# Optimization experiments

Hardware: AMD Instinct MI355X
Metric: run time of the kernel (lower is better)

## Reference

```python
import jax, jax.numpy as jnp
import numpy as np

H_OUT, W_OUT = 473, 473  # original image size the logits are upsampled to
BN_EPS = 1e-5


def _conv(x, w, pad):
    return jax.lax.conv_general_dilated(
        x, w, window_strides=(1, 1), padding=[(pad, pad), (pad, pad)],
        dimension_numbers=('NCHW', 'OIHW', 'NCHW'))


def _bn(x, g, b):
    # BatchNorm2d in training mode: batch statistics over (N, H, W)
    m = jnp.mean(x, axis=(0, 2, 3), keepdims=True)
    v = jnp.var(x, axis=(0, 2, 3), keepdims=True)
    return (x - m) * jax.lax.rsqrt(v + BN_EPS) * g.reshape(1, -1, 1, 1) + b.reshape(1, -1, 1, 1)


def setup_inputs() -> dict:
    key = jax.random.key(0)
    ks = jax.random.split(key, 8)
    B, C, Hf, Wf, NC = 2, 256, 60, 60, 2
    return {
        'V_a': jax.random.normal(ks[0], (B, C, Hf, Wf), jnp.float32),
        'V_b': jax.random.normal(ks[1], (B, C, Hf, Wf), jnp.float32),
        'D_a': jax.random.normal(ks[2], (B, C, Hf, Wf), jnp.float32),
        'W_e': jax.random.normal(ks[3], (C, C), jnp.float32) * 0.02,
        'gate_w': jax.random.normal(ks[4], (1, C, 1, 1), jnp.float32) * 0.01,
        'conv1_w': jax.random.normal(ks[5], (C, 3 * C, 3, 3), jnp.float32) * 0.01,
        'conv2_w': jax.random.normal(ks[6], (C, 2 * C, 3, 3), jnp.float32) * 0.01,
        'bn1_g': jnp.ones((C,), jnp.float32),
        'bn1_b': jnp.zeros((C,), jnp.float32),
        'bn2_g': jnp.ones((C,), jnp.float32),
        'bn2_b': jnp.zeros((C,), jnp.float32),
        'cls1_w': jax.random.normal(ks[7], (NC, C, 1, 1), jnp.float32) * 0.01,
        'cls1_b': jnp.zeros((NC,), jnp.float32),
        'cls2_w': jax.random.normal(jax.random.fold_in(key, 9), (NC, C, 1, 1), jnp.float32) * 0.01,
        'cls2_b': jnp.zeros((NC,), jnp.float32),
    }


def reference(V_a, V_b, D_a, W_e, gate_w, conv1_w, conv2_w,
              bn1_g, bn1_b, bn2_g, bn2_b, cls1_w, cls1_b, cls2_w, cls2_b):
    B, C, Hf, Wf = V_a.shape
    N = Hf * Wf
    V_a_flat = V_a.reshape(B, C, N)
    V_b_flat = V_b.reshape(B, C, N)

    # linear_e on transposed A features, then affinity S = (A^T W^T) B
    weighted = jnp.einsum('bcn,dc->bnd', V_a_flat, W_e)        # [B, N, C]
    S = jnp.einsum('bnd,bdm->bnm', weighted, V_b_flat)         # [B, N, N]

    S_row = jax.nn.softmax(S, axis=1)                          # softmax over dim 1
    S_colT = jax.nn.softmax(jnp.swapaxes(S, 1, 2), axis=1)     # softmax of S^T over dim 1

    Z_b = jnp.einsum('bcn,bnm->bcm', V_a_flat, S_row)          # attended for view b
    Z_a = jnp.einsum('bcn,bnm->bcm', V_b_flat, S_colT)         # attended for view a

    att1 = Z_a.reshape(B, C, Hf, Wf)
    att2 = Z_b.reshape(B, C, Hf, Wf)

    # 1x1 sigmoid gates
    att1 = att1 * jax.nn.sigmoid(_conv(att1, gate_w, 0))
    att2 = att2 * jax.nn.sigmoid(_conv(att2, gate_w, 0))

    # conc1: branch-1 concatenates gated attention, RGB feat, and depth feat
    x1 = jnp.concatenate([att1, V_a, D_a], axis=1)             # [B, 3C, Hf, Wf]
    x2 = jnp.concatenate([att2, V_b], axis=1)                  # [B, 2C, Hf, Wf]

    x1 = jax.nn.relu(_bn(_conv(x1, conv1_w, 1), bn1_g, bn1_b))
    x2 = jax.nn.relu(_bn(_conv(x2, conv2_w, 1), bn2_g, bn2_b))

    x1 = _conv(x1, cls1_w, 0) + cls1_b.reshape(1, -1, 1, 1)
    x2 = _conv(x2, cls2_w, 0) + cls2_b.reshape(1, -1, 1, 1)

    NC = cls1_w.shape[0]
    x1 = jax.image.resize(x1, (B, NC, H_OUT, W_OUT), 'linear')
    x2 = jax.image.resize(x2, (B, NC, H_OUT, W_OUT), 'linear')
    return jax.nn.sigmoid(x1), jax.nn.sigmoid(x2)
```

## Files before the change

### kernel.cpp

```cpp
#include <hip/hip_runtime.h>

#define BB 2
#define CC 256
#define NN 3600
#define NCH 2
#define HO 473
#define WO 473
#define NP 3648
#define NR 3712
#define LDT 72
#define NTI 29
#define ZKS 6

typedef unsigned short u16;
typedef __attribute__((ext_vector_type(8))) short short8;
typedef __attribute__((ext_vector_type(4))) float f32x4;

static __device__ __forceinline__ u16 f2bf(float f) {
    unsigned u = __float_as_uint(f);
    unsigned r = (u + 0x7FFF + ((u >> 16) & 1)) >> 16;
    return (u16)r;
}
static __device__ __forceinline__ u16 f2h(float f) {
    _Float16 h = (_Float16)f;
    return __builtin_bit_cast(unsigned short, h);
}
static __device__ __forceinline__ float h2f(u16 u) {
    _Float16 h = __builtin_bit_cast(_Float16, u);
    return (float)h;
}

__global__ __launch_bounds__(256)
void gemm_we(const u16* __restrict__ vat, const u16* __restrict__ web,
             u16* __restrict__ wgtb)
{
    __shared__ u16 As[128 * LDT];
    __shared__ u16 Bs[128 * LDT];
    const u16* A = vat + (long)blockIdx.z * NR * CC;
    u16* Cp = wgtb + (long)blockIdx.z * NR * CC;

    const int t = threadIdx.x;
    const int w = t >> 6, lane = t & 63;
    const int mh = (w >> 1) * 64, nh = (w & 1) * 64;
    const int lm = lane & 15, quad = lane >> 4;
    const int m0 = blockIdx.y * 128, n0 = blockIdx.x * 128;

    f32x4 acc[4][4] = {};

    for (int k0 = 0; k0 < CC; k0 += 64) {
#pragma unroll
        for (int i = 0; i < 4; ++i) {
            int idx = i * 256 + t;
            int row = idx >> 3, c8 = (idx & 7) * 8;
            int rg = m0 + row;
            uint4 v = make_uint4(0u, 0u, 0u, 0u);
            if (rg < NN) v = *(const uint4*)(A + (long)rg * CC + k0 + c8);
            *(uint4*)(&As[row * LDT + c8]) = v;
            uint4 bv = make_uint4(0u, 0u, 0u, 0u);
            if (n0 + row < CC) bv = *(const uint4*)(web + (long)(n0 + row) * CC + k0 + c8);
            *(uint4*)(&Bs[row * LDT + c8]) = bv;
        }
        __syncthreads();
#pragma unroll
        for (int s = 0; s < 2; ++s) {
            short8 a[4], b[4];
#pragma unroll
            for (int i = 0; i < 4; ++i)
                a[i] = *(const short8*)(&As[(mh + i * 16 + lm) * LDT + s * 32 + quad * 8]);
#pragma unroll
            for (int j = 0; j < 4; ++j)
                b[j] = *(const short8*)(&Bs[(nh + j * 16 + lm) * LDT + s * 32 + quad * 8]);
#pragma unroll
            for (int i = 0; i < 4; ++i)
#pragma unroll
                for (int j = 0; j < 4; ++j)
                    acc[i][j] = __builtin_amdgcn_mfma_f32_16x16x32_bf16(a[i], b[j], acc[i][j], 0, 0, 0);
        }
        __syncthreads();
    }
#pragma unroll
    for (int i = 0; i < 4; ++i)
#pragma unroll
        for (int r = 0; r < 4; ++r) {
            int row = m0 + mh + i * 16 + quad * 4 + r;
            if (row < NN)
#pragma unroll
                for (int j = 0; j < 4; ++j) {
                    int col = n0 + nh + j * 16 + lm;
                    if (col < CC) Cp[(long)row * CC + col] = f2bf(acc[i][j][r]);
                }
        }
}

__global__ __launch_bounds__(256)
void gemm_s_stats(const u16* __restrict__ A, const u16* __restrict__ B,
                  u16* __restrict__ Sh, u16* __restrict__ STh,
                  float* __restrict__ prowm, float* __restrict__ prows,
                  float* __restrict__ pcolm, float* __restrict__ pcols)
{
    __shared__ u16 smem[2 * 128 * LDT];
    u16* As = smem;
    u16* Bs = smem + 128 * LDT;

    const int t = threadIdx.x;
    const int w = t >> 6, lane = t & 63;
    const int mh = (w >> 1) * 64, nh = (w & 1) * 64;
    const int lm = lane & 15, quad = lane >> 4;
    const int m0 = blockIdx.y * 128, n0 = blockIdx.x * 128;

    f32x4 acc[4][4] = {};

    for (int k0 = 0; k0 < CC; k0 += 64) {
#pragma unroll
        for (int i = 0; i < 4; ++i) {
            int idx = i * 256 + t;
            int row = idx >> 3, c8 = (idx & 7) * 8;
            uint4 v = make_uint4(0u, 0u, 0u, 0u);
            if (m0 + row < NN) v = *(const uint4*)(A + (long)(m0 + row) * CC + k0 + c8);
            *(uint4*)(&As[row * LDT + c8]) = v;
            uint4 bv = make_uint4(0u, 0u, 0u, 0u);
            if (n0 + row < NN) bv = *(const uint4*)(B + (long)(n0 + row) * CC + k0 + c8);
            *(uint4*)(&Bs[row * LDT + c8]) = bv;
        }
        __syncthreads();
#pragma unroll
        for (int s = 0; s < 2; ++s) {
            short8 a[4], b[4];
#pragma unroll
            for (int i = 0; i < 4; ++i)
                a[i] = *(const short8*)(&As[(mh + i * 16 + lm) * LDT + s * 32 + quad * 8]);
#pragma unroll
            for (int j = 0; j < 4; ++j)
                b[j] = *(const short8*)(&Bs[(nh + j * 16 + lm) * LDT + s * 32 + quad * 8]);
#pragma unroll
            for (int i = 0; i < 4; ++i)
#pragma unroll
                for (int j = 0; j < 4; ++j)
                    acc[i][j] = __builtin_amdgcn_mfma_f32_16x16x32_bf16(a[i], b[j], acc[i][j], 0, 0, 0);
        }
        __syncthreads();
    }

#pragma unroll
    for (int i = 0; i < 4; ++i)
#pragma unroll
        for (int r = 0; r < 4; ++r) {
            int row = m0 + mh + i * 16 + quad * 4 + r;
            if (row < NN)
#pragma unroll
                for (int j = 0; j < 4; ++j) {
                    int col = n0 + nh + j * 16 + lm;
                    if (col < NN) Sh[(long)row * NP + col] = f2h(acc[i][j][r]);
                }
        }

    bool cval[4];
#pragma unroll
    for (int j = 0; j < 4; ++j) cval[j] = (n0 + nh + j * 16 + lm) < NN;

    float* sm = (float*)smem;
    float* rowm = sm;
    float* rows_ = sm + 256;
    float* colm = sm + 512;
    float* cols_ = sm + 768;
    __syncthreads();

#pragma unroll
    for (int i = 0; i < 4; ++i)
#pragma unroll
        for (int r = 0; r < 4; ++r) {
            float m = -3.0e38f;
#pragma unroll
            for (int j = 0; j < 4; ++j) if (cval[j]) m = fmaxf(m, acc[i][j][r]);
            m = fmaxf(m, __shfl_xor(m, 1, 64));
            m = fmaxf(m, __shfl_xor(m, 2, 64));
            m = fmaxf(m, __shfl_xor(m, 4, 64));
            m = fmaxf(m, __shfl_xor(m, 8, 64));
            float s = 0.f;
#pragma unroll
            for (int j = 0; j < 4; ++j) if (cval[j]) s += __expf(acc[i][j][r] - m);
            s += __shfl_xor(s, 1, 64);
            s += __shfl_xor(s, 2, 64);
            s += __shfl_xor(s, 4, 64);
            s += __shfl_xor(s, 8, 64);
            if (lm == 0) {
                int rr = mh + i * 16 + quad * 4 + r;
                rowm[(w & 1) * 128 + rr] = m;
                rows_[(w & 1) * 128 + rr] = s;
            }
        }

#pragma unroll
    for (int j = 0; j < 4; ++j) {
        float m = -3.0e38f;
#pragma unroll
        for (int i = 0; i < 4; ++i)
#pragma unroll
            for (int r = 0; r < 4; ++r)
                if (m0 + mh + i * 16 + quad * 4 + r < NN) m = fmaxf(m, acc[i][j][r]);
        m = fmaxf(m, __shfl_xor(m, 16, 64));
        m = fmaxf(m, __shfl_xor(m, 32, 64));
        float s = 0.f;
#pragma unroll
        for (int i = 0; i < 4; ++i)
#pragma unroll
            for (int r = 0; r < 4; ++r)
                if (m0 + mh + i * 16 + quad * 4 + r < NN) s += __expf(acc[i][j][r] - m);
        s += __shfl_xor(s, 16, 64);
        s += __shfl_xor(s, 32, 64);
        if (quad == 0) {
            int ccl = nh + j * 16 + lm;
            colm[(w >> 1) * 128 + ccl] = m;
            cols_[(w >> 1) * 128 + ccl] = s;
        }
    }
    __syncthreads();

    if (t < 128) {
        float m1 = rowm[t], m2 = rowm[128 + t];
        float M = fmaxf(m1, m2);
        float s = rows_[t] * __expf(m1 - M) + rows_[128 + t] * __expf(m2 - M);
        if (m0 + t < NN) {
            prowm[(long)blockIdx.x * NR + m0 + t] = M;
            prows[(long)blockIdx.x * NR + m0 + t] = s;
        }
    } else {
        int c = t - 128;
        float m1 = colm[c], m2 = colm[128 + c];
        float M = fmaxf(m1, m2);
        float s = cols_[c] * __expf(m1 - M) + cols_[128 + c] * __expf(m2 - M);
        if (n0 + c < NN) {
            pcolm[(long)blockIdx.y * NR + n0 + c] = M;
            pcols[(long)blockIdx.y * NR + n0 + c] = s;
        }
    }

    __syncthreads();
    u16* tr = smem;
#pragma unroll
    for (int i = 0; i < 4; ++i)
#pragma unroll
        for (int j = 0; j < 4; ++j)
#pragma unroll
            for (int r = 0; r < 4; ++r)
                tr[(nh + j * 16 + lm) * 136 + (mh + i * 16 + quad * 4 + r)] = f2h(acc[i][j][r]);
    __syncthreads();
    {
        int row = t >> 1, hf = t & 1;
        int mg = n0 + row;
        if (mg < NN) {
#pragma unroll
            for (int q = 0; q < 8; ++q) {
                int cb = m0 + hf * 64 + q * 8;
                if (cb < NN)
                    *(uint4*)(&STh[(long)mg * NP + cb]) =
                        *(const uint4*)(&tr[row * 136 + hf * 64 + q * 8]);
            }
        }
    }
}

__global__ __launch_bounds__(256)
void stats_combine(const float* __restrict__ prowm, const float* __restrict__ prows,
                   const float* __restrict__ pcolm, const float* __restrict__ pcols,
                   float* __restrict__ rmx, float* __restrict__ rsm,
                   float* __restrict__ cmx, float* __restrict__ csm)
{
    int i = blockIdx.x * 256 + threadIdx.x;
    if (i >= NN) return;
    const float* pm = blockIdx.y ? pcolm : prowm;
    const float* ps = blockIdx.y ? pcols : prows;
    float m = -3.0e38f, s = 0.f;
#pragma unroll 4
    for (int tI = 0; tI < NTI; ++tI) {
        float m2 = pm[(long)tI * NR + i], s2 = ps[(long)tI * NR + i];
        float M = fmaxf(m, m2);
        s = s * __expf(m - M) + s2 * __expf(m2 - M);
        m = M;
    }
    if (blockIdx.y) { cmx[i] = m; csm[i] = s; }
    else            { rmx[i] = m; rsm[i] = s; }
}

__global__ __launch_bounds__(256)
void p_build(u16* __restrict__ Sh, u16* __restrict__ STh,
             const float* __restrict__ rmx, const float* __restrict__ rsm,
             const float* __restrict__ cmx, const float* __restrict__ csm)
{
    int r = blockIdx.x;
    u16* M = blockIdx.y ? STh : Sh;
    const float* mx = blockIdx.y ? cmx : rmx;
    const float* sm = blockIdx.y ? csm : rsm;
    float mv = mx[r];
    float inv = 1.f / sm[r];
    u16* row = M + (long)r * NP;
    int t = threadIdx.x;
    for (int c0 = t * 8; c0 < NP; c0 += 2048) {
        uint4 hv = *(const uint4*)(row + c0);
        const u16* hp = (const u16*)&hv;
        u16 o[8];
#pragma unroll
        for (int e = 0; e < 8; ++e) {
            int c = c0 + e;
            o[e] = (c < NN) ? f2bf(__expf(h2f(hp[e]) - mv) * inv) : (u16)0;
        }
        *(uint4*)(row + c0) = *(const uint4*)o;
    }
}

__global__ __launch_bounds__(256, 4)
void gemm_z_128(const u16* __restrict__ vab_b, const u16* __restrict__ vbb_b,
                const u16* __restrict__ PT, const u16* __restrict__ P,
                float* __restrict__ Zb_b, float* __restrict__ Za_b)
{
    __shared__ u16 As[128 * LDT];
    __shared__ u16 Bs[128 * LDT];

    const int t = threadIdx.x;
    const int w = t >> 6, lane = t & 63;
    const int mh = (w >> 1) * 64, nh = (w & 1) * 64;
    const int lm = lane & 15, quad = lane >> 4;
    const int n0 = blockIdx.x * 128;
    const int ks = blockIdx.y;
    const int zz = blockIdx.z;
    const int branch = zz & 1;
    const int m0 = (zz >> 1) * 128;
    const u16* A = branch ? vbb_b : vab_b;
    const u16* B = branch ? P : PT;
    float* Cp = branch ? Za_b : Zb_b;

    const int base = 57 / ZKS, rem = 57 % ZKS;
    const int it0 = ks * base + (ks < rem ? ks : rem);
    const int itn = base + (ks < rem ? 1 : 0);

    f32x4 acc[4][4] = {};

    for (int it = it0; it < it0 + itn; ++it) {
        const int k0 = it * 64;
#pragma unroll
        for (int i = 0; i < 4; ++i) {
            int idx = i * 256 + t;
            int row = idx >> 3, c8 = (idx & 7) * 8;
            uint4 v = *(const uint4*)(A + (long)(m0 + row) * NP + k0 + c8);
            *(uint4*)(&As[row * LDT + c8]) = v;
            int rg = n0 + row;
            uint4 bv = make_uint4(0u, 0u, 0u, 0u);
            if (rg < NN) bv = *(const uint4*)(B + (long)rg * NP + k0 + c8);
            *(uint4*)(&Bs[row * LDT + c8]) = bv;
        }
        __syncthreads();
#pragma unroll
        for (int s = 0; s < 2; ++s) {
            short8 a[4], b[4];
#pragma unroll
            for (int i = 0; i < 4; ++i)
                a[i] = *(const short8*)(&As[(mh + i * 16 + lm) * LDT + s * 32 + quad * 8]);
#pragma unroll
            for (int j = 0; j < 4; ++j)
                b[j] = *(const short8*)(&Bs[(nh + j * 16 + lm) * LDT + s * 32 + quad * 8]);
#pragma unroll
            for (int i = 0; i < 4; ++i)
#pragma unroll
                for (int j = 0; j < 4; ++j)
                    acc[i][j] = __builtin_amdgcn_mfma_f32_16x16x32_bf16(a[i], b[j], acc[i][j], 0, 0, 0);
        }
        __syncthreads();
    }

#pragma unroll
    for (int i = 0; i < 4; ++i)
#pragma unroll
        for (int r = 0; r < 4; ++r) {
            int row = m0 + mh + i * 16 + quad * 4 + r;
#pragma unroll
            for (int j = 0; j < 4; ++j) {
                int col = n0 + nh + j * 16 + lm;
                if (col < NN)
                    atomicAdd(&Cp[(long)row * NN + col], acc[i][j][r]);
            }
        }
}

__global__ __launch_bounds__(256, 4)
void conv_both(const u16* __restrict__ W1, const u16* __restrict__ W2,
               const u16* __restrict__ gzaT, const u16* __restrict__ vat,
               const u16* __restrict__ daT, const u16* __restrict__ gzbT,
               const u16* __restrict__ vbt,
               float* __restrict__ y1, float* __restrict__ y2)
{
    __shared__ u16 As[128 * LDT];
    __shared__ u16 Bs[128 * LDT];

    const int t = threadIdx.x;
    const int w = t >> 6, lane = t & 63;
    const int mh = (w >> 1) * 64, nh = (w & 1) * 64;
    const int lm = lane & 15, quad = lane >> 4;

    const long L = blockIdx.x + (long)NTI * (blockIdx.y + (long)ZKS * blockIdx.z);
    const int combo = (int)(L & 7);
    const long rest = L >> 3;
    const int ks = (int)(rest % ZKS);
    const int px = (int)(rest / ZKS);
    const int which = combo >> 2;
    const int b = (combo >> 1) & 1;
    const int m0 = (combo & 1) * 128;
    const int n0 = px * 128;

    const int CIN = which ? 512 : 768;
    const int KT = 9 * CIN;
    const u16* W = which ? W2 : W1;
    const u16* P0 = which ? gzbT : gzaT;
    const u16* P1 = which ? vbt : vat;
    const u16* P2 = which ? vbt : daT;
    float* Y = which ? y2 : y1;
    const long pstride = (long)NR * CC;

    const int per = (KT / 64) / ZKS;
    const int it0 = ks * per;

    f32x4 acc[4][4] = {};

    for (int it = it0; it < it0 + per; ++it) {
        const int k0 = it * 64;
        int tap = k0 / CIN;
        int kloc = k0 - tap * CIN;
        int plane = kloc >> 8, cip = kloc & 255;
        int dh = tap / 3 - 1, dw = tap - (tap / 3) * 3 - 1;
        int off = dh * 60 + dw;
        const u16* src = (plane == 0) ? P0 : ((plane == 1) ? P1 : P2);
        src += (long)b * pstride + cip;

#pragma unroll
        for (int i = 0; i < 4; ++i) {
            int idx = i * 256 + t;
            int row = idx >> 3, c8 = (idx & 7) * 8;
            uint4 v = *(const uint4*)(W + (long)(m0 + row) * KT + k0 + c8);
            *(uint4*)(&As[row * LDT + c8]) = v;
            int p = n0 + row;
            uint4 bv = make_uint4(0u, 0u, 0u, 0u);
            if (p < NN) {
                int h = p / 60, wp = p - h * 60;
                int hh = h + dh, wq = wp + dw;
                if (hh >= 0 && hh < 60 && wq >= 0 && wq < 60)
                    bv = *(const uint4*)(src + (long)(p + off) * CC + c8);
            }
            *(uint4*)(&Bs[row * LDT + c8]) = bv;
        }
        __syncthreads();
#pragma unroll
        for (int s = 0; s < 2; ++s) {
            short8 a[4], bfr[4];
#pragma unroll
            for (int i = 0; i < 4; ++i)
                a[i] = *(const short8*)(&As[(mh + i * 16 + lm) * LDT + s * 32 + quad * 8]);
#pragma unroll
            for (int j = 0; j < 4; ++j)
                bfr[j] = *(const short8*)(&Bs[(nh + j * 16 + lm) * LDT + s * 32 + quad * 8]);
#pragma unroll
            for (int i = 0; i < 4; ++i)
#pragma unroll
                for (int j = 0; j < 4; ++j)
                    acc[i][j] = __builtin_amdgcn_mfma_f32_16x16x32_bf16(a[i], bfr[j], acc[i][j], 0, 0, 0);
        }
        __syncthreads();
    }

    float* out = Y + (long)b * CC * NN;
#pragma unroll
    for (int i = 0; i < 4; ++i)
#pragma unroll
        for (int r = 0; r < 4; ++r) {
            int row = m0 + mh + i * 16 + quad * 4 + r;
#pragma unroll
            for (int j = 0; j < 4; ++j) {
                int col = n0 + nh + j * 16 + lm;
                if (col < NN)
                    atomicAdd(&out[(long)row * NN + col], acc[i][j][r]);
            }
        }
}

__global__ __launch_bounds__(256)
void cvt_we(const float* __restrict__ W, u16* __restrict__ O)
{
    int i = blockIdx.x * 256 + threadIdx.x;
    if (i < CC * CC) O[i] = f2bf(W[i]);
}

__global__ __launch_bounds__(256)
void transpose_cvt(const float* __restrict__ V, u16* __restrict__ VT,
                   u16* __restrict__ Vpad)
{
    __shared__ float tile[64][65];
    int b = blockIdx.z, c0 = blockIdx.y * 64, n0 = blockIdx.x * 64;
    int t = threadIdx.x;
#pragma unroll
    for (int e = 0; e < 16; ++e) {
        int f = e * 256 + t; int i = f >> 6, j = f & 63;
        int n = n0 + j;
        float v = 0.f;
        if (n < NN) v = V[((long)b * CC + c0 + i) * NN + n];
        tile[i][j] = v;
        if (Vpad) Vpad[((long)b * CC + c0 + i) * NP + n] = f2bf(v);
    }
    __syncthreads();
#pragma unroll
    for (int e = 0; e < 16; ++e) {
        int f = e * 256 + t; int i = f >> 6, j = f & 63;
        int n = n0 + i;
        if (n < NN) VT[((long)b * NR + n) * CC + c0 + j] = f2bf(tile[j][i]);
    }
}

__global__ __launch_bounds__(256)
void transpose_gate(const float* __restrict__ Z, const float* __restrict__ sg,
                    u16* __restrict__ ZT)
{
    __shared__ float tile[64][65];
    int b = blockIdx.z, c0 = blockIdx.y * 64, n0 = blockIdx.x * 64;
    int t = threadIdx.x;
#pragma unroll
    for (int e = 0; e < 16; ++e) {
        int f = e * 256 + t; int i = f >> 6, j = f & 63;
        int n = n0 + j;
        float v = 0.f;
        if (n < NN) v = Z[((long)b * CC + c0 + i) * NN + n];
        tile[i][j] = v;
    }
    __syncthreads();
#pragma unroll
    for (int e = 0; e < 16; ++e) {
        int f = e * 256 + t; int i = f >> 6, j = f & 63;
        int n = n0 + i;
        if (n < NN)
            ZT[((long)b * NR + n) * CC + c0 + j] = f2bf(tile[j][i] * sg[b * NN + n]);
    }
}

template<int CIN>
__global__ __launch_bounds__(256)
void cvt_convw(const float* __restrict__ W, u16* __restrict__ O)
{
    const int KT = 9 * CIN;
    long idx = (long)blockIdx.x * 256 + threadIdx.x;
    if (idx >= (long)CC * KT) return;
    int co = (int)(idx / KT);
    int r = (int)(idx % KT);
    int tap = r / CIN, ci = r % CIN;
    O[idx] = f2bf(W[((long)co * CIN + ci) * 9 + tap]);
}

__global__ __launch_bounds__(256)
void gate_sig(const float* __restrict__ Z, const float* __restrict__ gw,
              float* __restrict__ sg)
{
    int t = threadIdx.x;
    int px = t & 63, ck = t >> 6;
    int b = blockIdx.y;
    int p = blockIdx.x * 64 + px;
    const float* Zp = Z + (long)b * CC * NN;
    float g = 0.f;
    if (p < NN) {
        for (int c = ck * 64; c < ck * 64 + 64; ++c) g += gw[c] * Zp[(long)c * NN + p];
    }
    __shared__ float red[256];
    red[t] = g;
    __syncthreads();
    if (t < 64) {
        int pp = blockIdx.x * 64 + t;
        if (pp < NN) {
            float tot = red[t] + red[t + 64] + red[t + 128] + red[t + 192];
            sg[b * NN + pp] = 1.f / (1.f + __expf(-tot));
        }
    }
}

__global__ __launch_bounds__(256)
void bn_stats_kernel(const float* __restrict__ Y, const float* __restrict__ g,
                     const float* __restrict__ beta, float* __restrict__ scale,
                     float* __restrict__ shift)
{
    int c = blockIdx.x, t = threadIdx.x;
    float s = 0.f, sq = 0.f;
    for (int b = 0; b < BB; ++b) {
        const float* p = Y + (long)b * CC * NN + (long)c * NN;
        for (int i = t; i < NN; i += 256) { float v = p[i]; s += v; sq += v * v; }
    }
    __shared__ float ls[256], lq[256];
    ls[t] = s; lq[t] = sq;
    __syncthreads();
    for (int off = 128; off > 0; off >>= 1) {
        if (t < off) { ls[t] += ls[t + off]; lq[t] += lq[t + off]; }
        __syncthreads();
    }
    if (t == 0) {
        const float inv = 1.f / (float)(BB * NN);
        float mean = ls[0] * inv;
        float var = fmaxf(lq[0] * inv - mean * mean, 0.f);
        float sc = g[c] * rsqrtf(var + 1e-5f);
        scale[c] = sc;
        shift[c] = beta[c] - mean * sc;
    }
}

__global__ __launch_bounds__(256)
void cls_kernel(const float* __restrict__ Y, const float* __restrict__ scale,
                const float* __restrict__ shift, const float* __restrict__ cw,
                const float* __restrict__ cb, float* __restrict__ O)
{
    int t = threadIdx.x;
    int px = t & 63, ck = t >> 6;
    int b = blockIdx.y;
    int p = blockIdx.x * 64 + px;
    const float* Yb = Y + (long)b * CC * NN;
    float a0 = 0.f, a1 = 0.f;
    if (p < NN) {
        for (int c = ck * 64; c < ck * 64 + 64; ++c) {
            float v = Yb[(long)c * NN + p] * scale[c] + shift[c];
            v = fmaxf(v, 0.f);
            a0 += cw[c] * v;
            a1 += cw[CC + c] * v;
        }
    }
    __shared__ float r0[256], r1[256];
    r0[t] = a0; r1[t] = a1;
    __syncthreads();
    if (t < 64) {
        int pp = blockIdx.x * 64 + t;
        if (pp < NN) {
            float s0 = r0[t] + r0[t + 64] + r0[t + 128] + r0[t + 192];
            float s1 = r1[t] + r1[t + 64] + r1[t + 128] + r1[t + 192];
            O[(long)b * NCH * NN + pp] = s0 + cb[0];
            O[(long)b * NCH * NN + NN + pp] = s1 + cb[1];
        }
    }
}

__global__ __launch_bounds__(256)
void resize_sig_kernel(const float* __restrict__ I1, const float* __restrict__ I2,
                       float* __restrict__ O)
{
    const long HALF = (long)BB * NCH * HO * WO;
    long gid = (long)blockIdx.x * 256 + threadIdx.x;
    if (gid >= HALF) return;
    int half = blockIdx.y;
    const float* I = half ? I2 : I1;
    float* Op = O + half * HALF;

    int j = (int)(gid % WO);
    long r = gid / WO;
    int i = (int)(r % HO);
    int pc = (int)(r / HO);
    const float* ip = I + (long)pc * NN;

    const float SCL = 60.0f / 473.0f;
    float fy = (i + 0.5f) * SCL - 0.5f;
    float fx = (j + 0.5f) * SCL - 0.5f;
    int y0 = (int)floorf(fy);
    int x0 = (int)floorf(fx);
    float ty = fy - (float)y0;
    float tx = fx - (float)x0;
    int y0c = max(y0, 0), y1c = min(y0 + 1, 59);
    int x0c = max(x0, 0), x1c = min(x0 + 1, 59);
    float va = ip[y0c * 60 + x0c], vb = ip[y0c * 60 + x1c];
    float vc = ip[y1c * 60 + x0c], vd = ip[y1c * 60 + x1c];
    float v = (1.f - ty) * ((1.f - tx) * va + tx * vb) + ty * ((1.f - tx) * vc + tx * vd);
    Op[gid] = 1.f / (1.f + __expf(-v));
}

extern "C" void kernel_launch(void* const* d_in, const int* in_sizes, int n_in,
                              void* d_out, int out_size, void* d_ws, size_t ws_size,
                              hipStream_t stream)
{
    const float* V_a    = (const float*)d_in[0];
    const float* V_b    = (const float*)d_in[1];
    const float* D_a    = (const float*)d_in[2];
    const float* W_e    = (const float*)d_in[3];
    const float* gate_w = (const float*)d_in[4];
    const float* conv1_w = (const float*)d_in[5];
    const float* conv2_w = (const float*)d_in[6];
    const float* bn1_g = (const float*)d_in[7];
    const float* bn1_b = (const float*)d_in[8];
    const float* bn2_g = (const float*)d_in[9];
    const float* bn2_b = (const float*)d_in[10];
    const float* cls1_w = (const float*)d_in[11];
    const float* cls1_b = (const float*)d_in[12];
    const float* cls2_w = (const float*)d_in[13];
    const float* cls2_b = (const float*)d_in[14];
    float* out = (float*)d_out;

    size_t off = 0;
    char* wsb = (char*)d_ws;
    auto carve = [&](size_t bytes) -> char* {
        char* p = wsb + off; off += (bytes + 255) & ~(size_t)255; return p;
    };

    u16* Sh    = (u16*)carve((size_t)NN * NP * 2);
    u16* STh   = (u16*)carve((size_t)NN * NP * 2);
    u16* vab   = (u16*)carve((size_t)BB * CC * NP * 2);
    u16* vbb   = (u16*)carve((size_t)BB * CC * NP * 2);
    u16* vat   = (u16*)carve((size_t)BB * NR * CC * 2);
    u16* vbt   = (u16*)carve((size_t)BB * NR * CC * 2);
    u16* daT   = (u16*)carve((size_t)BB * NR * CC * 2);
    u16* gzaT  = (u16*)carve((size_t)BB * NR * CC * 2);
    u16* gzbT  = (u16*)carve((size_t)BB * NR * CC * 2);
    u16* wgtb  = (u16*)carve((size_t)BB * NR * CC * 2);
    u16* web   = (u16*)carve((size_t)CC * CC * 2);
    u16* wt1   = (u16*)carve((size_t)CC * 9 * 768 * 2);
    u16* wt2   = (u16*)carve((size_t)CC * 9 * 512 * 2);
    float* Za  = (float*)carve((size_t)BB * CC * NN * 4);
    float* Zb  = (float*)carve((size_t)BB * CC * NN * 4);
    float* y1  = (float*)carve((size_t)BB * CC * NN * 4);
    float* y2  = (float*)carve((size_t)BB * CC * NN * 4);
    float* rmx = (float*)carve((size_t)BB * NN * 4);
    float* rsm = (float*)carve((size_t)BB * NN * 4);
    float* cmx = (float*)carve((size_t)BB * NN * 4);
    float* csm = (float*)carve((size_t)BB * NN * 4);
    float* sga = (float*)carve((size_t)BB * NN * 4);
    float* sgb = (float*)carve((size_t)BB * NN * 4);
    float* prm = (float*)carve((size_t)NTI * NR * 4);
    float* prs = (float*)carve((size_t)NTI * NR * 4);
    float* pcm = (float*)carve((size_t)NTI * NR * 4);
    float* pcs = (float*)carve((size_t)NTI * NR * 4);
    float* c1o = (float*)carve((size_t)BB * NCH * NN * 4);
    float* c2o = (float*)carve((size_t)BB * NCH * NN * 4);

    dim3 blk(256);

    hipMemsetAsync(Za, 0, (size_t)4 * BB * CC * NN * 4, stream);

    cvt_we<<<256, blk, 0, stream>>>(W_e, web);
    transpose_cvt<<<dim3(57, 4, BB), blk, 0, stream>>>(V_a, vat, vab);
    transpose_cvt<<<dim3(57, 4, BB), blk, 0, stream>>>(V_b, vbt, vbb);
    transpose_cvt<<<dim3(57, 4, BB), blk, 0, stream>>>(D_a, daT, nullptr);
    cvt_convw<768><<<(int)(((long)CC * 9 * 768 + 255) / 256), blk, 0, stream>>>(conv1_w, wt1);
    cvt_convw<512><<<(int)(((long)CC * 9 * 512 + 255) / 256), blk, 0, stream>>>(conv2_w, wt2);

    gemm_we<<<dim3(2, NTI, BB), blk, 0, stream>>>(vat, web, wgtb);

    for (int b = 0; b < BB; ++b) {
        const u16* wgtb_b = wgtb + (long)b * NR * CC;
        const u16* vbt_b  = vbt + (long)b * NR * CC;
        const u16* vab_b  = vab + (long)b * CC * NP;
        const u16* vbb_b  = vbb + (long)b * CC * NP;
        float* rmx_b = rmx + b * NN; float* rsm_b = rsm + b * NN;
        float* cmx_b = cmx + b * NN; float* csm_b = csm + b * NN;

        gemm_s_stats<<<dim3(NTI, NTI), blk, 0, stream>>>(
            wgtb_b, vbt_b, Sh, STh, prm, prs, pcm, pcs);
        stats_combine<<<dim3((NN + 255) / 256, 2), blk, 0, stream>>>(
            prm, prs, pcm, pcs, rmx_b, rsm_b, cmx_b, csm_b);
        p_build<<<dim3(NN, 2), blk, 0, stream>>>(Sh, STh, rmx_b, rsm_b, cmx_b, csm_b);
        gemm_z_128<<<dim3(NTI, ZKS, 4), blk, 0, stream>>>(
            vab_b, vbb_b, STh, Sh,
            Zb + (long)b * CC * NN, Za + (long)b * CC * NN);
    }

    gate_sig<<<dim3(57, BB), blk, 0, stream>>>(Za, gate_w, sga);
    gate_sig<<<dim3(57, BB), blk, 0, stream>>>(Zb, gate_w, sgb);
    transpose_gate<<<dim3(57, 4, BB), blk, 0, stream>>>(Za, sga, gzaT);
    transpose_gate<<<dim3(57, 4, BB), blk, 0, stream>>>(Zb, sgb, gzbT);

    conv_both<<<dim3(NTI, ZKS, 8), blk, 0, stream>>>(
        wt1, wt2, gzaT, vat, daT, gzbT, vbt, y1, y2);

    bn_stats_kernel<<<256, blk, 0, stream>>>(y1, bn1_g, bn1_b, rmx, rsm);
    bn_stats_kernel<<<256, blk, 0, stream>>>(y2, bn2_g, bn2_b, cmx, csm);
    cls_kernel<<<dim3(57, BB), blk, 0, stream>>>(y1, rmx, rsm, cls1_w, cls1_b, c1o);
    cls_kernel<<<dim3(57, BB), blk, 0, stream>>>(y2, cmx, csm, cls2_w, cls2_b, c2o);

    resize_sig_kernel<<<dim3((int)(((long)BB * NCH * HO * WO + 255) / 256), 2), blk, 0, stream>>>(c1o, c2o, out);
}
```

Measured before the change: 671.2 us.

## Prefetch next B tile into registers across three MFMA GEMM kernels

In the S-affinity GEMM, the attention-apply GEMM and the implicit-GEMM conv kernel, the B-operand global loads for the next k-step are now issued into registers before the current step's MFMA loop. This hides some global-memory latency behind compute. Per-thread row pointers, validity flags and conv pixel coordinates are hoisted out of the k-loop, and the trailing barrier moves to the top of each iteration. The cost is higher register pressure, which could reduce occupancy, especially for conv_both with launch bounds of 4 blocks per SM.

After: 814.5 us. +21.4%, slower.

```diff
diff --git a/kernel.cpp b/kernel.cpp
--- a/kernel.cpp
+++ b/kernel.cpp
@@ -108,21 +108,51 @@
     const int lm = lane & 15, quad = lane >> 4;
     const int m0 = blockIdx.y * 128, n0 = blockIdx.x * 128;
 
+    int rowv[4], c8v[4];
+    bool avalid[4], bvalid[4];
+    const u16* Arow[4];
+    const u16* Brow[4];
+#pragma unroll
+    for (int i = 0; i < 4; ++i) {
+        int idx = i * 256 + t;
+        int row = idx >> 3, c8 = (idx & 7) * 8;
+        rowv[i] = row; c8v[i] = c8;
+        avalid[i] = (m0 + row) < NN;
+        bvalid[i] = (n0 + row) < NN;
+        Arow[i] = A + (long)(m0 + row) * CC + c8;
+        Brow[i] = B + (long)(n0 + row) * CC + c8;
+    }
+
     f32x4 acc[4][4] = {};
-
+    uint4 pb[4];
+
+    auto issueB = [&](int k0) {
+#pragma unroll
+        for (int i = 0; i < 4; ++i) {
+            uint4 bv = make_uint4(0u, 0u, 0u, 0u);
+            if (bvalid[i]) bv = *(const uint4*)(Brow[i] + k0);
+            pb[i] = bv;
+        }
+    };
+
+    issueB(0);
     for (int k0 = 0; k0 < CC; k0 += 64) {
+        __syncthreads();
+        uint4 av[4];
 #pragma unroll
         for (int i = 0; i < 4; ++i) {
-            int idx = i * 256 + t;
-            int row = idx >> 3, c8 = (idx & 7) * 8;
             uint4 v = make_uint4(0u, 0u, 0u, 0u);
-            if (m0 + row < NN) v = *(const uint4*)(A + (long)(m0 + row) * CC + k0 + c8);
-            *(uint4*)(&As[row * LDT + c8]) = v;
-            uint4 bv = make_uint4(0u, 0u, 0u, 0u);
-            if (n0 + row < NN) bv = *(const uint4*)(B + (long)(n0 + row) * CC + k0 + c8);
-            *(uint4*)(&Bs[row * LDT + c8]) = bv;
-        }
+            if (avalid[i]) v = *(const uint4*)(Arow[i] + k0);
+            av[i] = v;
+        }
+#pragma unroll
+        for (int i = 0; i < 4; ++i)
+            *(uint4*)(&Bs[rowv[i] * LDT + c8v[i]]) = pb[i];
+#pragma unroll
+        for (int i = 0; i < 4; ++i)
+            *(uint4*)(&As[rowv[i] * LDT + c8v[i]]) = av[i];
         __syncthreads();
+        if (k0 + 64 < CC) issueB(k0 + 64);
 #pragma unroll
         for (int s = 0; s < 2; ++s) {
             short8 a[4], b[4];
@@ -138,7 +168,6 @@
                 for (int j = 0; j < 4; ++j)
                     acc[i][j] = __builtin_amdgcn_mfma_f32_16x16x32_bf16(a[i], b[j], acc[i][j], 0, 0, 0);
         }
-        __syncthreads();
     }
 
 #pragma unroll
@@ -333,22 +362,49 @@
     const int it0 = ks * base + (ks < rem ? ks : rem);
     const int itn = base + (ks < rem ? 1 : 0);
 
+    int rowv[4], c8v[4];
+    bool bvalid[4];
+    const u16* Arow[4];
+    const u16* Brow[4];
+#pragma unroll
+    for (int i = 0; i < 4; ++i) {
+        int idx = i * 256 + t;
+        int row = idx >> 3, c8 = (idx & 7) * 8;
+        rowv[i] = row; c8v[i] = c8;
+        Arow[i] = A + (long)(m0 + row) * NP + c8;
+        bvalid[i] = (n0 + row) < NN;
+        Brow[i] = B + (long)(n0 + row) * NP + c8;
+    }
+
     f32x4 acc[4][4] = {};
-
+    uint4 pb[4];
+
+    auto issueB = [&](int it) {
+        const int k0 = it * 64;
+#pragma unroll
+        for (int i = 0; i < 4; ++i) {
+            uint4 bv = make_uint4(0u, 0u, 0u, 0u);
+            if (bvalid[i]) bv = *(const uint4*)(Brow[i] + k0);
+            pb[i] = bv;
+        }
+    };
+
+    issueB(it0);
     for (int it = it0; it < it0 + itn; ++it) {
         const int k0 = it * 64;
-#pragma unroll
-        for (int i = 0; i < 4; ++i) {
-            int idx = i * 256 + t;
-            int row = idx >> 3, c8 = (idx & 7) * 8;
-            uint4 v = *(const uint4*)(A + (long)(m0 + row) * NP + k0 + c8);
-            *(uint4*)(&As[row * LDT + c8]) = v;
-            int rg = n0 + row;
-            uint4 bv = make_uint4(0u, 0u, 0u, 0u);
-            if (rg < NN) bv = *(const uint4*)(B + (long)rg * NP + k0 + c8);
-            *(uint4*)(&Bs[row * LDT + c8]) = bv;
-        }
         __syncthreads();
+        uint4 av[4];
+#pragma unroll
+        for (int i = 0; i < 4; ++i)
+            av[i] = *(const uint4*)(Arow[i] + k0);
+#pragma unroll
+        for (int i = 0; i < 4; ++i)
+            *(uint4*)(&Bs[rowv[i] * LDT + c8v[i]]) = pb[i];
+#pragma unroll
+        for (int i = 0; i < 4; ++i)
+            *(uint4*)(&As[rowv[i] * LDT + c8v[i]]) = av[i];
+        __syncthreads();
+        if (it + 1 < it0 + itn) issueB(it + 1);
 #pragma unroll
         for (int s = 0; s < 2; ++s) {
             short8 a[4], b[4];
@@ -364,7 +420,6 @@
                 for (int j = 0; j < 4; ++j)
                     acc[i][j] = __builtin_amdgcn_mfma_f32_16x16x32_bf16(a[i], b[j], acc[i][j], 0, 0, 0);
         }
-        __syncthreads();
     }
 
 #pragma unroll
@@ -418,9 +473,23 @@
     const int per = (KT / 64) / ZKS;
     const int it0 = ks * per;
 
+    int rowv[4], c8v[4], hv[4], wpv[4];
+    const u16* Arow[4];
+#pragma unroll
+    for (int i = 0; i < 4; ++i) {
+        int idx = i * 256 + t;
+        int row = idx >> 3, c8 = (idx & 7) * 8;
+        rowv[i] = row; c8v[i] = c8;
+        Arow[i] = W + (long)(m0 + row) * KT + c8;
+        int p = n0 + row;
+        hv[i] = p / 60;
+        wpv[i] = p - hv[i] * 60;
+    }
+
     f32x4 acc[4][4] = {};
-
-    for (int it = it0; it < it0 + per; ++it) {
+    uint4 pb[4];
+
+    auto issueB = [&](int it) {
         const int k0 = it * 64;
         int tap = k0 / CIN;
         int kloc = k0 - tap * CIN;
@@ -429,24 +498,33 @@
         int off = dh * 60 + dw;
         const u16* src = (plane == 0) ? P0 : ((plane == 1) ? P1 : P2);
         src += (long)b * pstride + cip;
-
 #pragma unroll
         for (int i = 0; i < 4; ++i) {
-            int idx = i * 256 + t;
-            int row = idx >> 3, c8 = (idx & 7) * 8;
-            uint4 v = *(const uint4*)(W + (long)(m0 + row) * KT + k0 + c8);
-            *(uint4*)(&As[row * LDT + c8]) = v;
-            int p = n0 + row;
+            int p = n0 + rowv[i];
+            int hh = hv[i] + dh, wq = wpv[i] + dw;
             uint4 bv = make_uint4(0u, 0u, 0u, 0u);
-            if (p < NN) {
-                int h = p / 60, wp = p - h * 60;
-                int hh = h + dh, wq = wp + dw;
-                if (hh >= 0 && hh < 60 && wq >= 0 && wq < 60)
-                    bv = *(const uint4*)(src + (long)(p + off) * CC + c8);
-            }
-            *(uint4*)(&Bs[row * LDT + c8]) = bv;
-        }
+            if (p < NN && hh >= 0 && hh < 60 && wq >= 0 && wq < 60)
+                bv = *(const uint4*)(src + (long)(p + off) * CC + c8v[i]);
+            pb[i] = bv;
+        }
+    };
+
+    issueB(it0);
+    for (int it = it0; it < it0 + per; ++it) {
+        const int k0 = it * 64;
         __syncthreads();
+        uint4 av[4];
+#pragma unroll
+        for (int i = 0; i < 4; ++i)
+            av[i] = *(const uint4*)(Arow[i] + k0);
+#pragma unroll
+        for (int i = 0; i < 4; ++i)
+            *(uint4*)(&Bs[rowv[i] * LDT + c8v[i]]) = pb[i];
+#pragma unroll
+        for (int i = 0; i < 4; ++i)
+            *(uint4*)(&As[rowv[i] * LDT + c8v[i]]) = av[i];
+        __syncthreads();
+        if (it + 1 < it0 + per) issueB(it + 1);
 #pragma unroll
         for (int s = 0; s < 2; ++s) {
             short8 a[4], bfr[4];
@@ -462,7 +540,6 @@
                 for (int j = 0; j < 4; ++j)
                     acc[i][j] = __builtin_amdgcn_mfma_f32_16x16x32_bf16(a[i], bfr[j], acc[i][j], 0, 0, 0);
         }
-        __syncthreads();
     }
 
     float* out = Y + (long)b * CC * NN;
```

## Use direct global-to-LDS loads with XOR-swizzled tiles in all GEMM kernels

Applied to the files above, without the earlier changes.

Replaces register-staged global loads and LDS stores in the four MFMA GEMM kernels with global_load_lds 16-byte direct transfers. The padded LDT=72 layout gives way to an unpadded 64-wide tile with an XOR swizzle, to avoid LDS bank conflicts while skipping the VGPR round trip. Bounds checks are removed by zero-padding the workspace (a memset over the padded buffers, and larger S buffers). The conv kernel redirects out-of-bounds halo reads to a zero buffer. This adds an extra memset and depends on padded rows staying zero.

Result: faster. 625.1 us (-6.9%).

```diff
diff --git a/kernel.cpp b/kernel.cpp
--- a/kernel.cpp
+++ b/kernel.cpp
@@ -8,7 +8,6 @@
 #define WO 473
 #define NP 3648
 #define NR 3712
-#define LDT 72
 #define NTI 29
 #define ZKS 6
 
@@ -30,12 +29,19 @@
     return (float)h;
 }
 
+static __device__ __forceinline__ void glds16(const u16* g, u16* l) {
+    __builtin_amdgcn_global_load_lds(
+        (const __attribute__((address_space(1))) void*)g,
+        (__attribute__((address_space(3))) void*)l, 16, 0, 0);
+}
+
+
 __global__ __launch_bounds__(256)
 void gemm_we(const u16* __restrict__ vat, const u16* __restrict__ web,
              u16* __restrict__ wgtb)
 {
-    __shared__ u16 As[128 * LDT];
-    __shared__ u16 Bs[128 * LDT];
+    __shared__ u16 As[128 * 64];
+    __shared__ u16 Bs[128 * 64];
     const u16* A = vat + (long)blockIdx.z * NR * CC;
     u16* Cp = wgtb + (long)blockIdx.z * NR * CC;
 
@@ -44,6 +50,7 @@
     const int mh = (w >> 1) * 64, nh = (w & 1) * 64;
     const int lm = lane & 15, quad = lane >> 4;
     const int m0 = blockIdx.y * 128, n0 = blockIdx.x * 128;
+    const int wb = t & 192;
 
     f32x4 acc[4][4] = {};
 
@@ -51,14 +58,10 @@
 #pragma unroll
         for (int i = 0; i < 4; ++i) {
             int idx = i * 256 + t;
-            int row = idx >> 3, c8 = (idx & 7) * 8;
-            int rg = m0 + row;
-            uint4 v = make_uint4(0u, 0u, 0u, 0u);
-            if (rg < NN) v = *(const uint4*)(A + (long)rg * CC + k0 + c8);
-            *(uint4*)(&As[row * LDT + c8]) = v;
-            uint4 bv = make_uint4(0u, 0u, 0u, 0u);
-            if (n0 + row < CC) bv = *(const uint4*)(web + (long)(n0 + row) * CC + k0 + c8);
-            *(uint4*)(&Bs[row * LDT + c8]) = bv;
+            int row = idx >> 3;
+            int sc8 = ((idx ^ row) & 7) * 8;
+            glds16(A + (long)(m0 + row) * CC + k0 + sc8, &As[(i * 256 + wb) * 8]);
+            glds16(web + (long)(n0 + row) * CC + k0 + sc8, &Bs[(i * 256 + wb) * 8]);
         }
         __syncthreads();
 #pragma unroll
@@ -66,10 +69,10 @@
             short8 a[4], b[4];
 #pragma unroll
             for (int i = 0; i < 4; ++i)
-                a[i] = *(const short8*)(&As[(mh + i * 16 + lm) * LDT + s * 32 + quad * 8]);
+                a[i] = *(const short8*)(&As[(mh + i * 16 + lm) * 64 + ((s * 4 + quad) ^ (lm & 7)) * 8]);
 #pragma unroll
             for (int j = 0; j < 4; ++j)
-                b[j] = *(const short8*)(&Bs[(nh + j * 16 + lm) * LDT + s * 32 + quad * 8]);
+                b[j] = *(const short8*)(&Bs[(nh + j * 16 + lm) * 64 + ((s * 4 + quad) ^ (lm & 7)) * 8]);
 #pragma unroll
             for (int i = 0; i < 4; ++i)
 #pragma unroll
@@ -98,15 +101,16 @@
                   float* __restrict__ prowm, float* __restrict__ prows,
                   float* __restrict__ pcolm, float* __restrict__ pcols)
 {
-    __shared__ u16 smem[2 * 128 * LDT];
+    __shared__ u16 smem[17408];
     u16* As = smem;
-    u16* Bs = smem + 128 * LDT;
+    u16* Bs = smem + 8192;
 
     const int t = threadIdx.x;
     const int w = t >> 6, lane = t & 63;
     const int mh = (w >> 1) * 64, nh = (w & 1) * 64;
     const int lm = lane & 15, quad = lane >> 4;
     const int m0 = blockIdx.y * 128, n0 = blockIdx.x * 128;
+    const int wb = t & 192;
 
     f32x4 acc[4][4] = {};
 
@@ -114,13 +118,10 @@
 #pragma unroll
         for (int i = 0; i < 4; ++i) {
             int idx = i * 256 + t;
-            int row = idx >> 3, c8 = (idx & 7) * 8;
-            uint4 v = make_uint4(0u, 0u, 0u, 0u);
-            if (m0 + row < NN) v = *(const uint4*)(A + (long)(m0 + row) * CC + k0 + c8);
-            *(uint4*)(&As[row * LDT + c8]) = v;
-            uint4 bv = make_uint4(0u, 0u, 0u, 0u);
-            if (n0 + row < NN) bv = *(const uint4*)(B + (long)(n0 + row) * CC + k0 + c8);
-            *(uint4*)(&Bs[row * LDT + c8]) = bv;
+            int row = idx >> 3;
+            int sc8 = ((idx ^ row) & 7) * 8;
+            glds16(A + (long)(m0 + row) * CC + k0 + sc8, &As[(i * 256 + wb) * 8]);
+            glds16(B + (long)(n0 + row) * CC + k0 + sc8, &Bs[(i * 256 + wb) * 8]);
         }
         __syncthreads();
 #pragma unroll
@@ -128,10 +129,10 @@
             short8 a[4], b[4];
 #pragma unroll
             for (int i = 0; i < 4; ++i)
-                a[i] = *(const short8*)(&As[(mh + i * 16 + lm) * LDT + s * 32 + quad * 8]);
+                a[i] = *(const short8*)(&As[(mh + i * 16 + lm) * 64 + ((s * 4 + quad) ^ (lm & 7)) * 8]);
 #pragma unroll
             for (int j = 0; j < 4; ++j)
-                b[j] = *(const short8*)(&Bs[(nh + j * 16 + lm) * LDT + s * 32 + quad * 8]);
+                b[j] = *(const short8*)(&Bs[(nh + j * 16 + lm) * 64 + ((s * 4 + quad) ^ (lm & 7)) * 8]);
 #pragma unroll
             for (int i = 0; i < 4; ++i)
 #pragma unroll
@@ -313,8 +314,8 @@
                 const u16* __restrict__ PT, const u16* __restrict__ P,
                 float* __restrict__ Zb_b, float* __restrict__ Za_b)
 {
-    __shared__ u16 As[128 * LDT];
-    __shared__ u16 Bs[128 * LDT];
+    __shared__ u16 As[128 * 64];
+    __shared__ u16 Bs[128 * 64];
 
     const int t = threadIdx.x;
     const int w = t >> 6, lane = t & 63;
@@ -328,6 +329,7 @@
     const u16* A = branch ? vbb_b : vab_b;
     const u16* B = branch ? P : PT;
     float* Cp = branch ? Za_b : Zb_b;
+    const int wb = t & 192;
 
     const int base = 57 / ZKS, rem = 57 % ZKS;
     const int it0 = ks * base + (ks < rem ? ks : rem);
@@ -340,13 +342,10 @@
 #pragma unroll
         for (int i = 0; i < 4; ++i) {
             int idx = i * 256 + t;
-            int row = idx >> 3, c8 = (idx & 7) * 8;
-            uint4 v = *(const uint4*)(A + (long)(m0 + row) * NP + k0 + c8);
-            *(uint4*)(&As[row * LDT + c8]) = v;
-            int rg = n0 + row;
-            uint4 bv = make_uint4(0u, 0u, 0u, 0u);
-            if (rg < NN) bv = *(const uint4*)(B + (long)rg * NP + k0 + c8);
-            *(uint4*)(&Bs[row * LDT + c8]) = bv;
+            int row = idx >> 3;
+            int sc8 = ((idx ^ row) & 7) * 8;
+            glds16(A + (long)(m0 + row) * NP + k0 + sc8, &As[(i * 256 + wb) * 8]);
+            glds16(B + (long)(n0 + row) * NP + k0 + sc8, &Bs[(i * 256 + wb) * 8]);
         }
         __syncthreads();
 #pragma unroll
@@ -354,10 +353,10 @@
             short8 a[4], b[4];
 #pragma unroll
             for (int i = 0; i < 4; ++i)
-                a[i] = *(const short8*)(&As[(mh + i * 16 + lm) * LDT + s * 32 + quad * 8]);
+                a[i] = *(const short8*)(&As[(mh + i * 16 + lm) * 64 + ((s * 4 + quad) ^ (lm & 7)) * 8]);
 #pragma unroll
             for (int j = 0; j < 4; ++j)
-                b[j] = *(const short8*)(&Bs[(nh + j * 16 + lm) * LDT + s * 32 + quad * 8]);
+                b[j] = *(const short8*)(&Bs[(nh + j * 16 + lm) * 64 + ((s * 4 + quad) ^ (lm & 7)) * 8]);
 #pragma unroll
             for (int i = 0; i < 4; ++i)
 #pragma unroll
@@ -385,16 +384,17 @@
 void conv_both(const u16* __restrict__ W1, const u16* __restrict__ W2,
                const u16* __restrict__ gzaT, const u16* __restrict__ vat,
                const u16* __restrict__ daT, const u16* __restrict__ gzbT,
-               const u16* __restrict__ vbt,
+               const u16* __restrict__ vbt, const u16* __restrict__ zbuf,
                float* __restrict__ y1, float* __restrict__ y2)
 {
-    __shared__ u16 As[128 * LDT];
-    __shared__ u16 Bs[128 * LDT];
+    __shared__ u16 As[128 * 64];
+    __shared__ u16 Bs[128 * 64];
 
     const int t = threadIdx.x;
     const int w = t >> 6, lane = t & 63;
     const int mh = (w >> 1) * 64, nh = (w & 1) * 64;
     const int lm = lane & 15, quad = lane >> 4;
+    const int wb = t & 192;
 
     const long L = blockIdx.x + (long)NTI * (blockIdx.y + (long)ZKS * blockIdx.z);
     const int combo = (int)(L & 7);
@@ -418,6 +418,17 @@
     const int per = (KT / 64) / ZKS;
     const int it0 = ks * per;
 
+    int pv[4], hv[4], wv[4], sc8v[4];
+#pragma unroll
+    for (int i = 0; i < 4; ++i) {
+        int idx = i * 256 + t;
+        int row = idx >> 3;
+        sc8v[i] = ((idx ^ row) & 7) * 8;
+        pv[i] = n0 + row;
+        hv[i] = pv[i] / 60;
+        wv[i] = pv[i] - hv[i] * 60;
+    }
+
     f32x4 acc[4][4] = {};
 
     for (int it = it0; it < it0 + per; ++it) {
@@ -433,18 +444,11 @@
 #pragma unroll
         for (int i = 0; i < 4; ++i) {
             int idx = i * 256 + t;
-            int row = idx >> 3, c8 = (idx & 7) * 8;
-            uint4 v = *(const uint4*)(W + (long)(m0 + row) * KT + k0 + c8);
-            *(uint4*)(&As[row * LDT + c8]) = v;
-            int p = n0 + row;
-            uint4 bv = make_uint4(0u, 0u, 0u, 0u);
-            if (p < NN) {
-                int h = p / 60, wp = p - h * 60;
-                int hh = h + dh, wq = wp + dw;
-                if (hh >= 0 && hh < 60 && wq >= 0 && wq < 60)
-                    bv = *(const uint4*)(src + (long)(p + off) * CC + c8);
-            }
-            *(uint4*)(&Bs[row * LDT + c8]) = bv;
+            int row = idx >> 3;
+            glds16(W + (long)(m0 + row) * KT + k0 + sc8v[i], &As[(i * 256 + wb) * 8]);
+            bool ok = pv[i] < NN && (unsigned)(hv[i] + dh) < 60u && (unsigned)(wv[i] + dw) < 60u;
+            const u16* gs = ok ? src + (long)(pv[i] + off) * CC + sc8v[i] : zbuf;
+            glds16(gs, &Bs[(i * 256 + wb) * 8]);
         }
         __syncthreads();
 #pragma unroll
@@ -452,10 +456,10 @@
             short8 a[4], bfr[4];
 #pragma unroll
             for (int i = 0; i < 4; ++i)
-                a[i] = *(const short8*)(&As[(mh + i * 16 + lm) * LDT + s * 32 + quad * 8]);
+                a[i] = *(const short8*)(&As[(mh + i * 16 + lm) * 64 + ((s * 4 + quad) ^ (lm & 7)) * 8]);
 #pragma unroll
             for (int j = 0; j < 4; ++j)
-                bfr[j] = *(const short8*)(&Bs[(nh + j * 16 + lm) * LDT + s * 32 + quad * 8]);
+                bfr[j] = *(const short8*)(&Bs[(nh + j * 16 + lm) * 64 + ((s * 4 + quad) ^ (lm & 7)) * 8]);
 #pragma unroll
             for (int i = 0; i < 4; ++i)
 #pragma unroll
@@ -695,8 +699,8 @@
         char* p = wsb + off; off += (bytes + 255) & ~(size_t)255; return p;
     };
 
-    u16* Sh    = (u16*)carve((size_t)NN * NP * 2);
-    u16* STh   = (u16*)carve((size_t)NN * NP * 2);
+    u16* Sh    = (u16*)carve((size_t)NR * NP * 2);
+    u16* STh   = (u16*)carve((size_t)NR * NP * 2);
     u16* vab   = (u16*)carve((size_t)BB * CC * NP * 2);
     u16* vbb   = (u16*)carve((size_t)BB * CC * NP * 2);
     u16* vat   = (u16*)carve((size_t)BB * NR * CC * 2);
@@ -705,6 +709,7 @@
     u16* gzaT  = (u16*)carve((size_t)BB * NR * CC * 2);
     u16* gzbT  = (u16*)carve((size_t)BB * NR * CC * 2);
     u16* wgtb  = (u16*)carve((size_t)BB * NR * CC * 2);
+    u16* zbuf  = (u16*)carve(256);
     u16* web   = (u16*)carve((size_t)CC * CC * 2);
     u16* wt1   = (u16*)carve((size_t)CC * 9 * 768 * 2);
     u16* wt2   = (u16*)carve((size_t)CC * 9 * 512 * 2);
@@ -728,6 +733,7 @@
     dim3 blk(256);
 
     hipMemsetAsync(Za, 0, (size_t)4 * BB * CC * NN * 4, stream);
+    hipMemsetAsync(vat, 0, (size_t)6 * ((size_t)BB * NR * CC * 2) + 256, stream);
 
     cvt_we<<<256, blk, 0, stream>>>(W_e, web);
     transpose_cvt<<<dim3(57, 4, BB), blk, 0, stream>>>(V_a, vat, vab);
@@ -762,7 +768,7 @@
     transpose_gate<<<dim3(57, 4, BB), blk, 0, stream>>>(Zb, sgb, gzbT);
 
     conv_both<<<dim3(NTI, ZKS, 8), blk, 0, stream>>>(
-        wt1, wt2, gzaT, vat, daT, gzbT, vbt, y1, y2);
+        wt1, wt2, gzaT, vat, daT, gzbT, vbt, zbuf, y1, y2);
 
     bn_stats_kernel<<<256, blk, 0, stream>>>(y1, bn1_g, bn1_b, rmx, rsm);
     bn_stats_kernel<<<256, blk, 0, stream>>>(y2, bn2_g, bn2_b, cmx, csm);
```
